# Kernel optimization log

Hardware: AMD Instinct MI355X
Metric: run time of the kernel (lower is better)

## Reference

```python
import jax, jax.numpy as jnp
import numpy as np

E = 512
H = 8
D = E // H  # head_dims = 64
MAXREL = 512


def setup_inputs() -> dict:
    key = jax.random.key(0)
    ks = jax.random.split(key, 12)
    B, L = 4, 1024
    s_lin = float(np.sqrt(6.0 / (D + D)))  # xavier uniform for (D,D)
    s_fc = float(np.sqrt(6.0 / (E + E)))
    s_tab = float(np.sqrt(6.0 / (2 * MAXREL + 1 + D)))
    return {
        "query": jax.random.normal(ks[0], (B, L, E), jnp.float32),
        "key": jax.random.normal(ks[1], (B, L, E), jnp.float32),
        "value": jax.random.normal(ks[2], (B, L, E), jnp.float32),
        "mask": jax.random.randint(ks[3], (B, 1, 1, L), 0, 2, jnp.int32),
        "Wq": jax.random.uniform(ks[4], (D, D), jnp.float32, -s_lin, s_lin),
        "bq": jnp.zeros((D,), jnp.float32),
        "Wk": jax.random.uniform(ks[5], (D, D), jnp.float32, -s_lin, s_lin),
        "bk": jnp.zeros((D,), jnp.float32),
        "Wv": jax.random.uniform(ks[6], (D, D), jnp.float32, -s_lin, s_lin),
        "bv": jnp.zeros((D,), jnp.float32),
        "Wfc": jax.random.uniform(ks[7], (E, E), jnp.float32, -s_fc, s_fc),
        "bfc": jnp.zeros((E,), jnp.float32),
        "rel_k_table": jax.random.uniform(ks[8], (2 * MAXREL + 1, D), jnp.float32, -s_tab, s_tab),
        "rel_v_table": jax.random.uniform(ks[9], (2 * MAXREL + 1, D), jnp.float32, -s_tab, s_tab),
    }


def _rel_indices(length_q, length_k):
    dist = jnp.arange(length_k)[None, :] - jnp.arange(length_q)[:, None]
    return jnp.clip(dist, -MAXREL, MAXREL) + MAXREL  # [Q, K]


def reference(query, key, value, mask, Wq, bq, Wk, bk, Wv, bv, Wfc, bfc, rel_k_table, rel_v_table):
    B, Q, _ = query.shape
    K = key.shape[1]
    q = query.reshape(B, Q, H, D) @ Wq.T + bq  # per-head linear (same weights all heads)
    k = key.reshape(B, K, H, D) @ Wk.T + bk
    v = value.reshape(B, K, H, D) @ Wv.T + bv

    scores = jnp.einsum("bqhd,bkhd->bhqk", q, k)  # [B,H,Q,K]
    scores = jnp.where(mask == 0, jnp.float32(-1e20), scores)  # mask BEFORE bias & scale, as in source

    idx = _rel_indices(Q, K)
    a_key = rel_k_table[idx]    # [Q,K,D]
    a_val = rel_v_table[idx]    # [Q,K,D]
    scores = scores + jnp.einsum("bqhd,qkd->bhqk", q, a_key)

    attn = jax.nn.softmax(scores / jnp.sqrt(jnp.float32(D)), axis=-1)

    out = jnp.einsum("bhqk,bkhd->bqhd", attn, v)  # standard AV
    out = out + jnp.einsum("bhqk,qkd->bqhd", attn, a_val)  # relative-position value term
    out = out.reshape(B, Q, H * D)
    return out @ Wfc.T + bfc
```

## Files before the change

kernel.cpp:

```cpp
#include <hip/hip_runtime.h>
#include <math.h>

#define BB 4
#define LL 1024
#define EE 512
#define HH 8
#define DD 64
#define MAXREL 512

typedef unsigned short u16;
typedef __attribute__((ext_vector_type(8))) short bf16x8;
typedef __attribute__((ext_vector_type(4))) float f32x4;

__device__ __forceinline__ u16 f2bf(float f) {
    unsigned int u = __float_as_uint(f);
    unsigned int r = (u + 0x7FFFu + ((u >> 16) & 1u)) >> 16;
    return (u16)r;
}
__device__ __forceinline__ float bf2f(u16 b) {
    return __uint_as_float(((unsigned int)b) << 16);
}
__device__ __forceinline__ bf16x8 ldf8_bf(const float* p) {
    const float4 a = *(const float4*)(p);
    const float4 b = *(const float4*)(p + 4);
    bf16x8 r;
    r[0] = (short)f2bf(a.x); r[1] = (short)f2bf(a.y);
    r[2] = (short)f2bf(a.z); r[3] = (short)f2bf(a.w);
    r[4] = (short)f2bf(b.x); r[5] = (short)f2bf(b.y);
    r[6] = (short)f2bf(b.z); r[7] = (short)f2bf(b.w);
    return r;
}

#define MF(A, B, C) __builtin_amdgcn_mfma_f32_16x16x32_bf16((A), (B), (C), 0, 0, 0)
#define EXPSC 0.1803368801111244f

__global__ __launch_bounds__(256) void proj_mfma_kernel(
    const float* __restrict__ q_in, const float* __restrict__ k_in, const float* __restrict__ v_in,
    const float* __restrict__ Wq, const float* __restrict__ bq,
    const float* __restrict__ Wk, const float* __restrict__ bk,
    const float* __restrict__ Wv, const float* __restrict__ bv,
    u16* __restrict__ qb, u16* __restrict__ kb, u16* __restrict__ vtb)
{
    int bh = blockIdx.x; int b = bh >> 3; int h = bh & 7;
    int l0 = blockIdx.y * 64;
    int t = threadIdx.x; int w = t >> 6; int lane = t & 63;
    int lg = lane >> 4, lc = lane & 15;
    int lt = l0 + w * 16;

    bf16x8 wq[4][2], wk[4][2], wv[4][2];
    #pragma unroll
    for (int dt = 0; dt < 4; ++dt)
        #pragma unroll
        for (int kc = 0; kc < 2; ++kc) {
            int d = dt * 16 + lc, ko = kc * 32 + lg * 8;
            wq[dt][kc] = ldf8_bf(Wq + d * DD + ko);
            wk[dt][kc] = ldf8_bf(Wk + d * DD + ko);
            wv[dt][kc] = ldf8_bf(Wv + d * DD + ko);
        }
    size_t xrow = ((size_t)b * LL + lt + lc) * EE + h * DD;
    bf16x8 xq[2], xk[2], xv[2];
    #pragma unroll
    for (int kc = 0; kc < 2; ++kc) {
        int ko = kc * 32 + lg * 8;
        xq[kc] = ldf8_bf(q_in + xrow + ko);
        xk[kc] = ldf8_bf(k_in + xrow + ko);
        xv[kc] = ldf8_bf(v_in + xrow + ko);
    }

    f32x4 aq[4] = {}, ak[4] = {}, av[4] = {};
    #pragma unroll
    for (int dt = 0; dt < 4; ++dt) {
        aq[dt] = MF(wq[dt][0], xq[0], aq[dt]);
        aq[dt] = MF(wq[dt][1], xq[1], aq[dt]);
        ak[dt] = MF(wk[dt][0], xk[0], ak[dt]);
        ak[dt] = MF(wk[dt][1], xk[1], ak[dt]);
        av[dt] = MF(xv[0], wv[dt][0], av[dt]);
        av[dt] = MF(xv[1], wv[dt][1], av[dt]);
    }

    #pragma unroll
    for (int dt = 0; dt < 4; ++dt) {
        u16 tq[4], tk[4], tv[4];
        #pragma unroll
        for (int r = 0; r < 4; ++r) {
            int d = dt * 16 + lg * 4 + r;
            tq[r] = f2bf(aq[dt][r] + bq[d]);
            tk[r] = f2bf(ak[dt][r] + bk[d]);
            tv[r] = f2bf(av[dt][r] + bv[dt * 16 + lc]);
        }
        size_t o = ((size_t)bh * LL + lt + lc) * DD + dt * 16 + lg * 4;
        *(uint2*)&qb[o] = *(uint2*)tq;
        *(uint2*)&kb[o] = *(uint2*)tk;
        size_t ov = ((size_t)bh * DD + dt * 16 + lc) * LL + lt + lg * 4;
        *(uint2*)&vtb[ov] = *(uint2*)tv;
    }
}

__global__ __launch_bounds__(256) void prep_kernel(
    const float* __restrict__ relk, const float* __restrict__ relv, const float* __restrict__ Wfc,
    u16* __restrict__ relk_pad, u16* __restrict__ relvt_pad, u16* __restrict__ wfcb)
{
    int idx = blockIdx.x * 256 + threadIdx.x;
    if (idx < 2048 * DD) {
        int r = idx >> 6, d = idx & 63;
        int j = r - 512; j = j < 0 ? 0 : (j > 2 * MAXREL ? 2 * MAXREL : j);
        relk_pad[idx] = f2bf(relk[j * DD + d]);
        int dd = idx >> 11, c = idx & 2047;
        int j2 = c - 512; j2 = j2 < 0 ? 0 : (j2 > 2 * MAXREL ? 2 * MAXREL : j2);
        relvt_pad[idx] = f2bf(relv[j2 * DD + dd]);
    }
    if (idx < EE * EE) wfcb[idx] = f2bf(Wfc[idx]);
}

__global__ __launch_bounds__(256) void attn_mfma_kernel(
    const u16* __restrict__ qb, const u16* __restrict__ kb, const u16* __restrict__ vtb,
    const int* __restrict__ mask,
    const u16* __restrict__ relk_pad, const u16* __restrict__ relvt_pad,
    u16* __restrict__ attn_out)
{
    __shared__ __align__(16) char smem[57600];
    u16* Vts  = (u16*)(smem + 18432);
    u16* RVts = (u16*)(smem + 27648);
    float* lred = (float*)(smem + 57344);
    float* obuf = (float*)smem;

    int bh = blockIdx.x, b = bh >> 3, h = bh & 7;
    int q0 = blockIdx.y * 32;
    int t = threadIdx.x, lane = t & 63, w = t >> 6;
    int rw = w & 1, cw = w >> 1;
    int rbase = rw * 16, c0a = cw * 32;
    int lg = lane >> 4, lc = lane & 15;
    int ub = c0a - rbase + 16;
    size_t bhL = (size_t)bh * LL;
    const u16* kb_bh = kb + bhL * DD;
    const u16* vt_bh = vtb + (size_t)bh * DD * LL;
    const int* mk_b = mask + b * LL;
    u16* Pw  = (u16*)(smem + 43008) + w * 640;
    u16* Pqw = (u16*)(smem + 48128) + w * 1152;

    int sr0 = t >> 3, ss0 = (t & 7) * 8;
    int sr1 = sr0 + 32;
    int rv_row = t >> 2, rv_q = (t & 3) * 24;
    const u16* rvg = relvt_pad + (size_t)rv_row * 2048 + rv_q;
    u16* rvl = RVts + rv_row * 120 + rv_q;
    const u16* rk_base = relk_pad + (size_t)(ub + lc) * DD + lg * 8;

    const u16* qrow = qb + (bhL + q0 + rbase + lc) * DD;
    bf16x8 qf0 = *(const bf16x8*)&qrow[lg * 8];
    bf16x8 qf1 = *(const bf16x8*)&qrow[32 + lg * 8];

    f32x4 s0, s1, g0, g1, g2;
    bf16x8 rk0, rk1, rk2, rk3, rk4, rk5;
    f32x4 oacc[4] = {};
    float lacc[4] = {0.f, 0.f, 0.f, 0.f};
    int delta0 = lc - lg * 4;

#define LOAD_RK(SB) do { \
    const u16* rkp_ = rk_base + (size_t)(SB) * DD; \
    rk0 = *(const bf16x8*)&rkp_[0]; \
    rk1 = *(const bf16x8*)&rkp_[32]; \
    rk2 = *(const bf16x8*)&rkp_[16 * DD]; \
    rk3 = *(const bf16x8*)&rkp_[16 * DD + 32]; \
    rk4 = *(const bf16x8*)&rkp_[32 * DD]; \
    rk5 = *(const bf16x8*)&rkp_[32 * DD + 32]; \
} while (0)

#define DO_SCORES(KBASE) do { \
    const u16* kp0_ = (KBASE) + (c0a + lc) * 72; \
    const u16* kp1_ = (KBASE) + (c0a + 16 + lc) * 72; \
    s0 = (f32x4){0.f,0.f,0.f,0.f}; s1 = s0; g0 = s0; g1 = s0; g2 = s0; \
    __builtin_amdgcn_s_setprio(1); \
    s0 = MF(qf0, *(const bf16x8*)&kp0_[lg * 8], s0); \
    s0 = MF(qf1, *(const bf16x8*)&kp0_[32 + lg * 8], s0); \
    s1 = MF(qf0, *(const bf16x8*)&kp1_[lg * 8], s1); \
    s1 = MF(qf1, *(const bf16x8*)&kp1_[32 + lg * 8], s1); \
    g0 = MF(qf0, rk0, g0); g0 = MF(qf1, rk1, g0); \
    g1 = MF(qf0, rk2, g1); g1 = MF(qf1, rk3, g1); \
    g2 = MF(qf0, rk4, g2); g2 = MF(qf1, rk5, g2); \
    __builtin_amdgcn_s_setprio(0); \
} while (0)

#define DO_SOFTMAX(MB0, MB1) do { \
    _Pragma("unroll") \
    for (int r = 0; r < 4; ++r) { \
        int d_ = delta0 - r; \
        int src_ = (lane & 48) | (d_ & 15); \
        float a0_ = __shfl(g0[r], src_, 64); \
        float a1_ = __shfl(g1[r], src_, 64); \
        float a2_ = __shfl(g2[r], src_, 64); \
        float gv0_ = (d_ >= 0) ? a1_ : a0_; \
        float gv1_ = (d_ >= 0) ? a2_ : a1_; \
        float p0_ = exp2f((s0[r] + (MB0) + gv0_) * EXPSC); \
        float p1_ = exp2f((s1[r] + (MB1) + gv1_) * EXPSC); \
        u16 pb0_ = f2bf(p0_), pb1_ = f2bf(p1_); \
        lacc[r] += p0_ + p1_; \
        int row_ = lg * 4 + r; \
        Pw[row_ * 40 + lc] = pb0_; \
        Pw[row_ * 40 + 16 + lc] = pb1_; \
        Pqw[row_ * 72 + lc - row_ + 16] = pb0_; \
        Pqw[row_ * 72 + 32 + lc - row_] = pb1_; \
    } \
} while (0)

    #pragma unroll
    for (int i = 0; i < 3; ++i) {
        int u = lane + i * 64;
        if (u < 144) *(uint4*)&Pqw[u * 8] = make_uint4(0, 0, 0, 0);
    }
    if (t < 192) {
        int row = t / 3, j = t - row * 3;
        *(uint4*)&RVts[row * 120 + 96 + j * 8] = make_uint4(0, 0, 0, 0);
    }
    int sb0 = 992 - q0;
    {
        u16* Ks0 = (u16*)smem;
        u16* Ks1 = (u16*)(smem + 9216);
        *(uint4*)&Ks0[sr0 * 72 + ss0] = *(const uint4*)&kb_bh[(size_t)sr0 * DD + ss0];
        *(uint4*)&Ks0[sr1 * 72 + ss0] = *(const uint4*)&kb_bh[(size_t)sr1 * DD + ss0];
        *(uint4*)&Ks1[sr0 * 72 + ss0] = *(const uint4*)&kb_bh[(size_t)(64 + sr0) * DD + ss0];
        *(uint4*)&Ks1[sr1 * 72 + ss0] = *(const uint4*)&kb_bh[(size_t)(64 + sr1) * DD + ss0];
        *(uint4*)&Vts[sr0 * 72 + ss0] = *(const uint4*)&vt_bh[(size_t)sr0 * LL + ss0];
        *(uint4*)&Vts[sr1 * 72 + ss0] = *(const uint4*)&vt_bh[(size_t)sr1 * LL + ss0];
        *(uint4*)&rvl[0]  = *(const uint4*)&rvg[sb0];
        *(uint4*)&rvl[8]  = *(const uint4*)&rvg[sb0 + 8];
        *(uint4*)&rvl[16] = *(const uint4*)&rvg[sb0 + 16];
    }
    LOAD_RK(sb0);
    float mbp0 = (mk_b[c0a + lc] != 0) ? 0.f : -1e20f;
    float mbp1 = (mk_b[c0a + 16 + lc] != 0) ? 0.f : -1e20f;
    __syncthreads();
    DO_SCORES((const u16*)smem);
    LOAD_RK(sb0 + 64);
    DO_SOFTMAX(mbp0, mbp1);

    #pragma unroll 1
    for (int c = 0; c < 16; ++c) {
        int k0 = c * 64;
        int sb_ = k0 - q0 + 992;
        uint4 rK0, rK1, rV0, rV1;
        float mbn0 = 0.f, mbn1 = 0.f;
        if (c < 14) {
            rK0 = *(const uint4*)&kb_bh[(size_t)(k0 + 128 + sr0) * DD + ss0];
            rK1 = *(const uint4*)&kb_bh[(size_t)(k0 + 128 + sr1) * DD + ss0];
        }
        if (c < 15) {
            int k0n = k0 + 64;
            rV0 = *(const uint4*)&vt_bh[(size_t)sr0 * LL + k0n + ss0];
            rV1 = *(const uint4*)&vt_bh[(size_t)sr1 * LL + k0n + ss0];
            mbn0 = (mk_b[k0n + c0a + lc] != 0) ? 0.f : -1e20f;
            mbn1 = (mk_b[k0n + c0a + 16 + lc] != 0) ? 0.f : -1e20f;
        }

        bf16x8 pa  = *(const bf16x8*)&Pw[lc * 40 + lg * 8];
        bf16x8 pq0 = *(const bf16x8*)&Pqw[lc * 72 + lg * 8];
        bf16x8 pq1 = *(const bf16x8*)&Pqw[lc * 72 + 32 + lg * 8];

        if (c < 15) {
            const u16* kcur = (const u16*)(smem + ((c + 1) & 1) * 9216);
            DO_SCORES(kcur);
            if (c < 14) LOAD_RK(sb_ + 128);
        }

        __builtin_amdgcn_s_setprio(1);
        #pragma unroll
        for (int dt = 0; dt < 4; ++dt) {
            const u16* vp = &Vts[(dt * 16 + lc) * 72 + c0a];
            const u16* rp = &RVts[(dt * 16 + lc) * 120 + ub];
            oacc[dt] = MF(pa,  *(const bf16x8*)&vp[lg * 8], oacc[dt]);
            oacc[dt] = MF(pq0, *(const bf16x8*)&rp[lg * 8], oacc[dt]);
            oacc[dt] = MF(pq1, *(const bf16x8*)&rp[32 + lg * 8], oacc[dt]);
        }
        __builtin_amdgcn_s_setprio(0);

        if (c < 15) {
            DO_SOFTMAX(mbn0, mbn1);
            int sbn = sb_ + 64;
            uint4 bb0 = *(const uint4*)&rvg[sbn];
            uint4 bb1 = *(const uint4*)&rvg[sbn + 8];
            uint4 bb2 = *(const uint4*)&rvg[sbn + 16];
            __syncthreads();
            if (c < 14) {
                u16* kwr = (u16*)(smem + (c & 1) * 9216);
                *(uint4*)&kwr[sr0 * 72 + ss0] = rK0;
                *(uint4*)&kwr[sr1 * 72 + ss0] = rK1;
            }
            *(uint4*)&Vts[sr0 * 72 + ss0] = rV0;
            *(uint4*)&Vts[sr1 * 72 + ss0] = rV1;
            *(uint4*)&rvl[0]  = bb0;
            *(uint4*)&rvl[8]  = bb1;
            *(uint4*)&rvl[16] = bb2;
            __syncthreads();
        }
    }
#undef LOAD_RK
#undef DO_SCORES
#undef DO_SOFTMAX

    #pragma unroll
    for (int m2 = 1; m2 <= 8; m2 <<= 1) {
        #pragma unroll
        for (int r = 0; r < 4; ++r) lacc[r] += __shfl_xor(lacc[r], m2);
    }
    __syncthreads();
    if (lc == 0) {
        #pragma unroll
        for (int r = 0; r < 4; ++r) lred[cw * 32 + rbase + lg * 4 + r] = lacc[r];
    }
    __syncthreads();
    if (cw == 1) {
        #pragma unroll
        for (int dt = 0; dt < 4; ++dt)
            #pragma unroll
            for (int r = 0; r < 4; ++r)
                obuf[(rbase + lg * 4 + r) * 68 + dt * 16 + lc] = oacc[dt][r];
    }
    __syncthreads();
    if (cw == 0) {
        float inv[4];
        #pragma unroll
        for (int r = 0; r < 4; ++r) {
            int row = rbase + lg * 4 + r;
            inv[r] = 1.0f / (lred[row] + lred[32 + row]);
        }
        #pragma unroll
        for (int dt = 0; dt < 4; ++dt) {
            #pragma unroll
            for (int r = 0; r < 4; ++r) {
                int row = rbase + lg * 4 + r;
                float v = (oacc[dt][r] + obuf[row * 68 + dt * 16 + lc]) * inv[r];
                attn_out[((size_t)b * LL + q0 + row) * EE + h * DD + dt * 16 + lc] = f2bf(v);
            }
        }
    }
}

__global__ __launch_bounds__(256) void fc_mfma_kernel(
    const u16* __restrict__ Xb, const u16* __restrict__ Wb,
    const float* __restrict__ bfc, float* __restrict__ out)
{
    __shared__ u16 As[128][72];
    __shared__ u16 Bs[128][72];
    int m0 = blockIdx.x * 128, n0 = blockIdx.y * 128;
    int t = threadIdx.x, lane = t & 63, w = t >> 6;
    int rw = w & 1, cw = w >> 1;
    int lg = lane >> 4, lc = lane & 15;
    f32x4 acc[4][4] = {};

    for (int kt = 0; kt < EE; kt += 64) {
        __syncthreads();
        #pragma unroll
        for (int i = 0; i < 4; ++i) {
            int unit = i * 256 + t;
            int row = unit >> 3, s = unit & 7;
            *(uint4*)&As[row][s * 8] = *(const uint4*)&Xb[(size_t)(m0 + row) * EE + kt + s * 8];
            *(uint4*)&Bs[row][s * 8] = *(const uint4*)&Wb[(size_t)(n0 + row) * EE + kt + s * 8];
        }
        __syncthreads();
        #pragma unroll
        for (int kc = 0; kc < 2; ++kc) {
            bf16x8 af[4], bf[4];
            #pragma unroll
            for (int i = 0; i < 4; ++i) {
                af[i] = *(const bf16x8*)&As[rw * 64 + i * 16 + lc][kc * 32 + lg * 8];
                bf[i] = *(const bf16x8*)&Bs[cw * 64 + i * 16 + lc][kc * 32 + lg * 8];
            }
            #pragma unroll
            for (int mi = 0; mi < 4; ++mi)
                #pragma unroll
                for (int ni = 0; ni < 4; ++ni)
                    acc[mi][ni] = MF(af[mi], bf[ni], acc[mi][ni]);
        }
    }
    #pragma unroll
    for (int mi = 0; mi < 4; ++mi) {
        #pragma unroll
        for (int ni = 0; ni < 4; ++ni) {
            int n = n0 + cw * 64 + ni * 16 + lc;
            float bias = bfc[n];
            #pragma unroll
            for (int r = 0; r < 4; ++r) {
                int m = m0 + rw * 64 + mi * 16 + lg * 4 + r;
                out[(size_t)m * EE + n] = acc[mi][ni][r] + bias;
            }
        }
    }
}

extern "C" void kernel_launch(void* const* d_in, const int* in_sizes, int n_in,
                              void* d_out, int out_size, void* d_ws, size_t ws_size,
                              hipStream_t stream) {
    const float* query = (const float*)d_in[0];
    const float* key   = (const float*)d_in[1];
    const float* value = (const float*)d_in[2];
    const int*   mask  = (const int*)d_in[3];
    const float* Wq  = (const float*)d_in[4];
    const float* bq  = (const float*)d_in[5];
    const float* Wk  = (const float*)d_in[6];
    const float* bk  = (const float*)d_in[7];
    const float* Wv  = (const float*)d_in[8];
    const float* bv  = (const float*)d_in[9];
    const float* Wfc = (const float*)d_in[10];
    const float* bfc = (const float*)d_in[11];
    const float* relk = (const float*)d_in[12];
    const float* relv = (const float*)d_in[13];
    float* out = (float*)d_out;

    char* ws = (char*)d_ws;
    u16* qb        = (u16*)(ws);
    u16* kb        = (u16*)(ws + (4u << 20));
    u16* vtb       = (u16*)(ws + (8u << 20));
    u16* attnb     = (u16*)(ws + (12u << 20));
    u16* relk_pad  = (u16*)(ws + (16u << 20));
    u16* relvt_pad = (u16*)(ws + (16u << 20) + 262144);
    u16* wfcb      = (u16*)(ws + (16u << 20) + 524288);

    proj_mfma_kernel<<<dim3(BB * HH, LL / 64), 256, 0, stream>>>(
        query, key, value, Wq, bq, Wk, bk, Wv, bv, qb, kb, vtb);
    prep_kernel<<<1024, 256, 0, stream>>>(relk, relv, Wfc, relk_pad, relvt_pad, wfcb);
    attn_mfma_kernel<<<dim3(BB * HH, LL / 32), 256, 0, stream>>>(
        qb, kb, vtb, mask, relk_pad, relvt_pad, attnb);
    fc_mfma_kernel<<<dim3(BB * LL / 128, EE / 128), 256, 0, stream>>>(attnb, wfcb, bfc, out);
}
```

Baseline: 109.5 us.

## Merge prep into projection launch, single-buffer K in attention, shrink FC tile

The rel-table and Wfc bf16 conversion now runs in 128 extra blocks of the projection kernel, which removes one kernel launch. The attention kernel drops K double-buffering to cut LDS from about 57.6KB to 48KB, which may allow more resident blocks, and it issues the rel-V global loads earlier in the loop. Softmax probabilities are packed to bf16 with a single v_cvt_pk_bf16_f32 instruction. The FC GEMM tile is halved in M to launch more blocks. With a single K buffer the next K tile can only be written after a barrier, so load latency is less hidden.

```diff
diff --git a/kernel.cpp b/kernel.cpp
--- a/kernel.cpp
+++ b/kernel.cpp
@@ -16,9 +16,6 @@
     unsigned int u = __float_as_uint(f);
     unsigned int r = (u + 0x7FFFu + ((u >> 16) & 1u)) >> 16;
     return (u16)r;
-}
-__device__ __forceinline__ float bf2f(u16 b) {
-    return __uint_as_float(((unsigned int)b) << 16);
 }
 __device__ __forceinline__ bf16x8 ldf8_bf(const float* p) {
     const float4 a = *(const float4*)(p);
@@ -39,11 +36,31 @@
     const float* __restrict__ Wq, const float* __restrict__ bq,
     const float* __restrict__ Wk, const float* __restrict__ bk,
     const float* __restrict__ Wv, const float* __restrict__ bv,
-    u16* __restrict__ qb, u16* __restrict__ kb, u16* __restrict__ vtb)
+    const float* __restrict__ relk, const float* __restrict__ relv, const float* __restrict__ Wfc,
+    u16* __restrict__ qb, u16* __restrict__ kb, u16* __restrict__ vtb,
+    u16* __restrict__ relk_pad, u16* __restrict__ relvt_pad, u16* __restrict__ wfcb)
 {
+    int t = threadIdx.x;
+    if (blockIdx.x >= 32) {
+        int pid = (blockIdx.x - 32) * 16 + blockIdx.y;
+        #pragma unroll
+        for (int i = 0; i < 8; ++i) {
+            int idx = pid * 256 + i * 32768 + t;
+            if (idx < 2048 * DD) {
+                int r = idx >> 6, d = idx & 63;
+                int j = r - 512; j = j < 0 ? 0 : (j > 2 * MAXREL ? 2 * MAXREL : j);
+                relk_pad[idx] = f2bf(relk[j * DD + d]);
+                int dd = idx >> 11, c = idx & 2047;
+                int j2 = c - 512; j2 = j2 < 0 ? 0 : (j2 > 2 * MAXREL ? 2 * MAXREL : j2);
+                relvt_pad[idx] = f2bf(relv[j2 * DD + dd]);
+            }
+            wfcb[idx] = f2bf(Wfc[idx]);
+        }
+        return;
+    }
     int bh = blockIdx.x; int b = bh >> 3; int h = bh & 7;
     int l0 = blockIdx.y * 64;
-    int t = threadIdx.x; int w = t >> 6; int lane = t & 63;
+    int w = t >> 6; int lane = t & 63;
     int lg = lane >> 4, lc = lane & 15;
     int lt = l0 + w * 16;
 
@@ -96,32 +113,17 @@
     }
 }
 
-__global__ __launch_bounds__(256) void prep_kernel(
-    const float* __restrict__ relk, const float* __restrict__ relv, const float* __restrict__ Wfc,
-    u16* __restrict__ relk_pad, u16* __restrict__ relvt_pad, u16* __restrict__ wfcb)
-{
-    int idx = blockIdx.x * 256 + threadIdx.x;
-    if (idx < 2048 * DD) {
-        int r = idx >> 6, d = idx & 63;
-        int j = r - 512; j = j < 0 ? 0 : (j > 2 * MAXREL ? 2 * MAXREL : j);
-        relk_pad[idx] = f2bf(relk[j * DD + d]);
-        int dd = idx >> 11, c = idx & 2047;
-        int j2 = c - 512; j2 = j2 < 0 ? 0 : (j2 > 2 * MAXREL ? 2 * MAXREL : j2);
-        relvt_pad[idx] = f2bf(relv[j2 * DD + dd]);
-    }
-    if (idx < EE * EE) wfcb[idx] = f2bf(Wfc[idx]);
-}
-
 __global__ __launch_bounds__(256) void attn_mfma_kernel(
     const u16* __restrict__ qb, const u16* __restrict__ kb, const u16* __restrict__ vtb,
     const int* __restrict__ mask,
     const u16* __restrict__ relk_pad, const u16* __restrict__ relvt_pad,
     u16* __restrict__ attn_out)
 {
-    __shared__ __align__(16) char smem[57600];
-    u16* Vts  = (u16*)(smem + 18432);
-    u16* RVts = (u16*)(smem + 27648);
-    float* lred = (float*)(smem + 57344);
+    __shared__ __align__(16) char smem[48384];
+    u16* Ks   = (u16*)(smem);
+    u16* Vts  = (u16*)(smem + 9216);
+    u16* RVts = (u16*)(smem + 18432);
+    float* lred = (float*)(smem + 48128);
     float* obuf = (float*)smem;
 
     int bh = blockIdx.x, b = bh >> 3, h = bh & 7;
@@ -135,8 +137,8 @@
     const u16* kb_bh = kb + bhL * DD;
     const u16* vt_bh = vtb + (size_t)bh * DD * LL;
     const int* mk_b = mask + b * LL;
-    u16* Pw  = (u16*)(smem + 43008) + w * 640;
-    u16* Pqw = (u16*)(smem + 48128) + w * 1152;
+    u16* Pw  = (u16*)(smem + 33792) + w * 640;
+    u16* Pqw = (u16*)(smem + 38912) + w * 1152;
 
     int sr0 = t >> 3, ss0 = (t & 7) * 8;
     int sr1 = sr0 + 32;
@@ -165,9 +167,9 @@
     rk5 = *(const bf16x8*)&rkp_[32 * DD + 32]; \
 } while (0)
 
-#define DO_SCORES(KBASE) do { \
-    const u16* kp0_ = (KBASE) + (c0a + lc) * 72; \
-    const u16* kp1_ = (KBASE) + (c0a + 16 + lc) * 72; \
+#define DO_SCORES() do { \
+    const u16* kp0_ = Ks + (c0a + lc) * 72; \
+    const u16* kp1_ = Ks + (c0a + 16 + lc) * 72; \
     s0 = (f32x4){0.f,0.f,0.f,0.f}; s1 = s0; g0 = s0; g1 = s0; g2 = s0; \
     __builtin_amdgcn_s_setprio(1); \
     s0 = MF(qf0, *(const bf16x8*)&kp0_[lg * 8], s0); \
@@ -192,7 +194,9 @@
         float gv1_ = (d_ >= 0) ? a2_ : a1_; \
         float p0_ = exp2f((s0[r] + (MB0) + gv0_) * EXPSC); \
         float p1_ = exp2f((s1[r] + (MB1) + gv1_) * EXPSC); \
-        u16 pb0_ = f2bf(p0_), pb1_ = f2bf(p1_); \
+        unsigned pk_; \
+        asm("v_cvt_pk_bf16_f32 %0, %1, %2" : "=v"(pk_) : "v"(p0_), "v"(p1_)); \
+        u16 pb0_ = (u16)pk_, pb1_ = (u16)(pk_ >> 16); \
         lacc[r] += p0_ + p1_; \
         int row_ = lg * 4 + r; \
         Pw[row_ * 40 + lc] = pb0_; \
@@ -212,32 +216,34 @@
         *(uint4*)&RVts[row * 120 + 96 + j * 8] = make_uint4(0, 0, 0, 0);
     }
     int sb0 = 992 - q0;
-    {
-        u16* Ks0 = (u16*)smem;
-        u16* Ks1 = (u16*)(smem + 9216);
-        *(uint4*)&Ks0[sr0 * 72 + ss0] = *(const uint4*)&kb_bh[(size_t)sr0 * DD + ss0];
-        *(uint4*)&Ks0[sr1 * 72 + ss0] = *(const uint4*)&kb_bh[(size_t)sr1 * DD + ss0];
-        *(uint4*)&Ks1[sr0 * 72 + ss0] = *(const uint4*)&kb_bh[(size_t)(64 + sr0) * DD + ss0];
-        *(uint4*)&Ks1[sr1 * 72 + ss0] = *(const uint4*)&kb_bh[(size_t)(64 + sr1) * DD + ss0];
-        *(uint4*)&Vts[sr0 * 72 + ss0] = *(const uint4*)&vt_bh[(size_t)sr0 * LL + ss0];
-        *(uint4*)&Vts[sr1 * 72 + ss0] = *(const uint4*)&vt_bh[(size_t)sr1 * LL + ss0];
-        *(uint4*)&rvl[0]  = *(const uint4*)&rvg[sb0];
-        *(uint4*)&rvl[8]  = *(const uint4*)&rvg[sb0 + 8];
-        *(uint4*)&rvl[16] = *(const uint4*)&rvg[sb0 + 16];
-    }
+    *(uint4*)&Ks[sr0 * 72 + ss0] = *(const uint4*)&kb_bh[(size_t)sr0 * DD + ss0];
+    *(uint4*)&Ks[sr1 * 72 + ss0] = *(const uint4*)&kb_bh[(size_t)sr1 * DD + ss0];
+    *(uint4*)&Vts[sr0 * 72 + ss0] = *(const uint4*)&vt_bh[(size_t)sr0 * LL + ss0];
+    *(uint4*)&Vts[sr1 * 72 + ss0] = *(const uint4*)&vt_bh[(size_t)sr1 * LL + ss0];
+    *(uint4*)&rvl[0]  = *(const uint4*)&rvg[sb0];
+    *(uint4*)&rvl[8]  = *(const uint4*)&rvg[sb0 + 8];
+    *(uint4*)&rvl[16] = *(const uint4*)&rvg[sb0 + 16];
     LOAD_RK(sb0);
     float mbp0 = (mk_b[c0a + lc] != 0) ? 0.f : -1e20f;
     float mbp1 = (mk_b[c0a + 16 + lc] != 0) ? 0.f : -1e20f;
     __syncthreads();
-    DO_SCORES((const u16*)smem);
+    DO_SCORES();
     LOAD_RK(sb0 + 64);
     DO_SOFTMAX(mbp0, mbp1);
+    {
+        uint4 k1a = *(const uint4*)&kb_bh[(size_t)(64 + sr0) * DD + ss0];
+        uint4 k1b = *(const uint4*)&kb_bh[(size_t)(64 + sr1) * DD + ss0];
+        __syncthreads();
+        *(uint4*)&Ks[sr0 * 72 + ss0] = k1a;
+        *(uint4*)&Ks[sr1 * 72 + ss0] = k1b;
+        __syncthreads();
+    }
 
     #pragma unroll 1
     for (int c = 0; c < 16; ++c) {
         int k0 = c * 64;
         int sb_ = k0 - q0 + 992;
-        uint4 rK0, rK1, rV0, rV1;
+        uint4 rK0, rK1, rV0, rV1, rRV0, rRV1, rRV2;
         float mbn0 = 0.f, mbn1 = 0.f;
         if (c < 14) {
             rK0 = *(const uint4*)&kb_bh[(size_t)(k0 + 128 + sr0) * DD + ss0];
@@ -245,8 +251,12 @@
         }
         if (c < 15) {
             int k0n = k0 + 64;
-            rV0 = *(const uint4*)&vt_bh[(size_t)sr0 * LL + k0n + ss0];
-            rV1 = *(const uint4*)&vt_bh[(size_t)sr1 * LL + k0n + ss0];
+            int sbn = sb_ + 64;
+            rV0  = *(const uint4*)&vt_bh[(size_t)sr0 * LL + k0n + ss0];
+            rV1  = *(const uint4*)&vt_bh[(size_t)sr1 * LL + k0n + ss0];
+            rRV0 = *(const uint4*)&rvg[sbn];
+            rRV1 = *(const uint4*)&rvg[sbn + 8];
+            rRV2 = *(const uint4*)&rvg[sbn + 16];
             mbn0 = (mk_b[k0n + c0a + lc] != 0) ? 0.f : -1e20f;
             mbn1 = (mk_b[k0n + c0a + 16 + lc] != 0) ? 0.f : -1e20f;
         }
@@ -256,8 +266,7 @@
         bf16x8 pq1 = *(const bf16x8*)&Pqw[lc * 72 + 32 + lg * 8];
 
         if (c < 15) {
-            const u16* kcur = (const u16*)(smem + ((c + 1) & 1) * 9216);
-            DO_SCORES(kcur);
+            DO_SCORES();
             if (c < 14) LOAD_RK(sb_ + 128);
         }
 
@@ -274,21 +283,16 @@
 
         if (c < 15) {
             DO_SOFTMAX(mbn0, mbn1);
-            int sbn = sb_ + 64;
-            uint4 bb0 = *(const uint4*)&rvg[sbn];
-            uint4 bb1 = *(const uint4*)&rvg[sbn + 8];
-            uint4 bb2 = *(const uint4*)&rvg[sbn + 16];
             __syncthreads();
             if (c < 14) {
-                u16* kwr = (u16*)(smem + (c & 1) * 9216);
-                *(uint4*)&kwr[sr0 * 72 + ss0] = rK0;
-                *(uint4*)&kwr[sr1 * 72 + ss0] = rK1;
+                *(uint4*)&Ks[sr0 * 72 + ss0] = rK0;
+                *(uint4*)&Ks[sr1 * 72 + ss0] = rK1;
             }
             *(uint4*)&Vts[sr0 * 72 + ss0] = rV0;
             *(uint4*)&Vts[sr1 * 72 + ss0] = rV1;
-            *(uint4*)&rvl[0]  = bb0;
-            *(uint4*)&rvl[8]  = bb1;
-            *(uint4*)&rvl[16] = bb2;
+            *(uint4*)&rvl[0]  = rRV0;
+            *(uint4*)&rvl[8]  = rRV1;
+            *(uint4*)&rvl[16] = rRV2;
             __syncthreads();
         }
     }
@@ -338,48 +342,54 @@
     const u16* __restrict__ Xb, const u16* __restrict__ Wb,
     const float* __restrict__ bfc, float* __restrict__ out)
 {
-    __shared__ u16 As[128][72];
+    __shared__ u16 As[64][72];
     __shared__ u16 Bs[128][72];
-    int m0 = blockIdx.x * 128, n0 = blockIdx.y * 128;
+    int m0 = blockIdx.x * 64, n0 = blockIdx.y * 128;
     int t = threadIdx.x, lane = t & 63, w = t >> 6;
     int rw = w & 1, cw = w >> 1;
     int lg = lane >> 4, lc = lane & 15;
-    f32x4 acc[4][4] = {};
+    f32x4 acc[2][4] = {};
 
     for (int kt = 0; kt < EE; kt += 64) {
         __syncthreads();
+        #pragma unroll
+        for (int i = 0; i < 2; ++i) {
+            int unit = i * 256 + t;
+            int row = unit >> 3, s = unit & 7;
+            *(uint4*)&As[row][s * 8] = *(const uint4*)&Xb[(size_t)(m0 + row) * EE + kt + s * 8];
+        }
         #pragma unroll
         for (int i = 0; i < 4; ++i) {
             int unit = i * 256 + t;
             int row = unit >> 3, s = unit & 7;
-            *(uint4*)&As[row][s * 8] = *(const uint4*)&Xb[(size_t)(m0 + row) * EE + kt + s * 8];
             *(uint4*)&Bs[row][s * 8] = *(const uint4*)&Wb[(size_t)(n0 + row) * EE + kt + s * 8];
         }
         __syncthreads();
         #pragma unroll
         for (int kc = 0; kc < 2; ++kc) {
-            bf16x8 af[4], bf[4];
-            #pragma unroll
-            for (int i = 0; i < 4; ++i) {
-                af[i] = *(const bf16x8*)&As[rw * 64 + i * 16 + lc][kc * 32 + lg * 8];
+            bf16x8 af[2], bf[4];
+            #pragma unroll
+            for (int i = 0; i < 2; ++i)
+                af[i] = *(const bf16x8*)&As[rw * 32 + i * 16 + lc][kc * 32 + lg * 8];
+            #pragma unroll
+            for (int i = 0; i < 4; ++i)
                 bf[i] = *(const bf16x8*)&Bs[cw * 64 + i * 16 + lc][kc * 32 + lg * 8];
-            }
-            #pragma unroll
-            for (int mi = 0; mi < 4; ++mi)
+            #pragma unroll
+            for (int mi = 0; mi < 2; ++mi)
                 #pragma unroll
                 for (int ni = 0; ni < 4; ++ni)
                     acc[mi][ni] = MF(af[mi], bf[ni], acc[mi][ni]);
         }
     }
     #pragma unroll
-    for (int mi = 0; mi < 4; ++mi) {
+    for (int mi = 0; mi < 2; ++mi) {
         #pragma unroll
         for (int ni = 0; ni < 4; ++ni) {
             int n = n0 + cw * 64 + ni * 16 + lc;
             float bias = bfc[n];
             #pragma unroll
             for (int r = 0; r < 4; ++r) {
-                int m = m0 + rw * 64 + mi * 16 + lg * 4 + r;
+                int m = m0 + rw * 32 + mi * 16 + lg * 4 + r;
                 out[(size_t)m * EE + n] = acc[mi][ni][r] + bias;
             }
         }
@@ -414,10 +424,10 @@
     u16* relvt_pad = (u16*)(ws + (16u << 20) + 262144);
     u16* wfcb      = (u16*)(ws + (16u << 20) + 524288);
 
-    proj_mfma_kernel<<<dim3(BB * HH, LL / 64), 256, 0, stream>>>(
-        query, key, value, Wq, bq, Wk, bk, Wv, bv, qb, kb, vtb);
-    prep_kernel<<<1024, 256, 0, stream>>>(relk, relv, Wfc, relk_pad, relvt_pad, wfcb);
+    proj_mfma_kernel<<<dim3(40, LL / 64), 256, 0, stream>>>(
+        query, key, value, Wq, bq, Wk, bk, Wv, bv, relk, relv, Wfc,
+        qb, kb, vtb, relk_pad, relvt_pad, wfcb);
     attn_mfma_kernel<<<dim3(BB * HH, LL / 32), 256, 0, stream>>>(
         qb, kb, vtb, mask, relk_pad, relvt_pad, attnb);
-    fc_mfma_kernel<<<dim3(BB * LL / 128, EE / 128), 256, 0, stream>>>(attnb, wfcb, bfc, out);
-}
+    fc_mfma_kernel<<<dim3(BB * LL / 64, EE / 128), 256, 0, stream>>>(attnb, wfcb, bfc, out);
+}
```

After: 111.4 us. About the same (+1.7%).
